# Kernel optimization log

Hardware: AMD Instinct MI355X
Metric: run time of the kernel (lower is better)

Reference implementation:

```python
import jax, jax.numpy as jnp
import numpy as np

N = 100000
E = 1600000
EPS = 1e-5
NEG_SLOPE = 0.01


def _leaky(x):
    return jnp.where(x > 0, x, NEG_SLOPE * x)


def _conv2d(x, w, b):
    # x: [N,Cin,H,W], w: [Cout,Cin,kh,kw], VALID padding, stride 1
    y = jax.lax.conv_general_dilated(x, w, (1, 1), 'VALID',
                                     dimension_numbers=('NCHW', 'OIHW', 'NCHW'))
    return y + b[None, :, None, None]


def _bn(x, g, b, m, v):
    # eval-mode BatchNorm1d over feature dim
    return (x - m) * (g / jnp.sqrt(v + EPS)) + b


def setup_inputs() -> dict:
    key = jax.random.key(0)
    ks = jax.random.split(key, 64)
    d = {}
    d['inputs'] = jax.random.normal(ks[0], (N, 1, 100, 5), dtype=jnp.float32)
    d['edge_index'] = jax.random.randint(ks[1], (2, E), 0, N, dtype=jnp.int32)
    # CNN encoder params (x=10)
    d['cw1'] = 0.1 * jax.random.normal(ks[2], (10, 1, 3, 3), dtype=jnp.float32)
    d['cb1'] = jnp.zeros((10,), jnp.float32)
    d['cw2'] = 0.1 * jax.random.normal(ks[3], (20, 10, 3, 2), dtype=jnp.float32)
    d['cb2'] = jnp.zeros((20,), jnp.float32)
    d['cw3'] = 0.1 * jax.random.normal(ks[4], (1, 20, 3, 2), dtype=jnp.float32)
    d['cb3'] = jnp.zeros((1,), jnp.float32)
    dims = [94, 128, 128, 64, 64, 16]
    for i in range(5):
        fi, fo = dims[i], dims[i + 1]
        k = 8 + 4 * i
        d[f'gw{i+1}'] = jax.random.normal(ks[k], (fi, fo), jnp.float32) / np.sqrt(fi)
        d[f'gb{i+1}'] = jnp.zeros((fo,), jnp.float32)
        d[f'bn{i+1}_g'] = 1.0 + 0.1 * jax.random.normal(ks[k + 1], (fo,), jnp.float32)
        d[f'bn{i+1}_b'] = 0.1 * jax.random.normal(ks[k + 2], (fo,), jnp.float32)
        d[f'bn{i+1}_m'] = 0.1 * jax.random.normal(ks[k + 3], (fo,), jnp.float32)
        d[f'bn{i+1}_v'] = jax.random.uniform(ks[k + 3], (fo,), jnp.float32, 0.5, 1.5)
    return d


def reference(inputs, edge_index,
              cw1, cb1, cw2, cb2, cw3, cb3,
              gw1, gb1, gw2, gb2, gw3, gb3, gw4, gb4, gw5, gb5,
              bn1_g, bn1_b, bn1_m, bn1_v,
              bn2_g, bn2_b, bn2_m, bn2_v,
              bn3_g, bn3_b, bn3_m, bn3_v,
              bn4_g, bn4_b, bn4_m, bn4_v,
              bn5_g, bn5_b, bn5_m, bn5_v):
    n = inputs.shape[0]
    # --- GCN normalization (self-loops + symmetric deg^-1/2) ---
    loops = jnp.arange(n, dtype=edge_index.dtype)
    src = jnp.concatenate([edge_index[0], loops])
    dst = jnp.concatenate([edge_index[1], loops])
    deg = jax.ops.segment_sum(jnp.ones_like(src, dtype=jnp.float32), dst, num_segments=n)
    dinv = jnp.where(deg > 0, jax.lax.rsqrt(deg), 0.0)
    norm = dinv[src] * dinv[dst]  # [E+N]

    def gcn(h, w, b):
        m = (h @ w)[src] * norm[:, None]
        return jax.ops.segment_sum(m, dst, num_segments=n) + b

    # --- CNN encoder (dropout identity in eval) ---
    h = _conv2d(inputs, cw1, cb1)
    h = _leaky(h)
    h = _conv2d(h, cw2, cb2)
    h = _leaky(h)
    h = _conv2d(h, cw3, cb3)  # [N,1,94,1]
    h = jnp.tanh(h.reshape(-1, 94))

    h = jnp.tanh(_bn(gcn(h, gw1, gb1), bn1_g, bn1_b, bn1_m, bn1_v))
    h = jnp.tanh(_bn(gcn(h, gw2, gb2), bn2_g, bn2_b, bn2_m, bn2_v))
    h = jnp.tanh(_bn(gcn(h, gw3, gb3), bn3_g, bn3_b, bn3_m, bn3_v))
    h = jnp.tanh(_bn(gcn(h, gw4, gb4), bn4_g, bn4_b, bn4_m, bn4_v))
    h = _bn(gcn(h, gw5, gb5), bn5_g, bn5_b, bn5_m, bn5_v)
    return jax.nn.softmax(h, axis=1)
```

## Files before the change

### kernel.cpp

```cpp
#include <hip/hip_runtime.h>
#include <math.h>

namespace {

constexpr int NN = 100000;
constexpr int NE = 1600000;
constexpr float EPS = 1e-5f;

__device__ __forceinline__ float leaky(float x) { return fmaxf(x, 0.01f * x); }
__device__ __forceinline__ float ffma(float a, float b, float c) { return __builtin_fmaf(a, b, c); }


__global__ __launch_bounds__(256) void k_init(int* __restrict__ deg, int* __restrict__ counter, int n) {
  int i = blockIdx.x * 256 + threadIdx.x;
  if (i < n) deg[i] = 1;
  if (i == 0) counter[0] = 0;
}

__global__ __launch_bounds__(256) void k_count(const int* __restrict__ dst, int* __restrict__ deg, int e) {
  int i = blockIdx.x * 256 + threadIdx.x;
  if (i < e) atomicAdd(&deg[dst[i]], 1);
}

__global__ __launch_bounds__(256) void k_alloc(const int* __restrict__ deg, float* __restrict__ dinv,
                                               int* __restrict__ offsets, int* __restrict__ cursor,
                                               int* __restrict__ counter, int n) {
  int i = blockIdx.x * 256 + threadIdx.x;
  int lane = threadIdx.x & 63;
  int c = 0;
  if (i < n) {
    int d = deg[i];
    dinv[i] = rsqrtf((float)d);
    c = d - 1;
  }
  int v = c;
#pragma unroll
  for (int s = 1; s < 64; s <<= 1) {
    int t = __shfl_up(v, s, 64);
    if (lane >= s) v += t;
  }
  int total = __shfl(v, 63, 64);
  int base = 0;
  if (lane == 63) base = atomicAdd(counter, total);
  base = __shfl(base, 63, 64);
  if (i < n) {
    int off = base + v - c;
    offsets[i] = off;
    cursor[i] = off;
  }
}

__global__ __launch_bounds__(256) void k_fill(const int* __restrict__ src, const int* __restrict__ dst,
                                              const float* __restrict__ dinv, int* __restrict__ cursor,
                                              int2* __restrict__ adj, int e) {
  int i = blockIdx.x * 256 + threadIdx.x;
  if (i < e) {
    int s = src[i], d = dst[i];
    int p = atomicAdd(&cursor[d], 1);
    adj[p] = make_int2(s, __float_as_int(dinv[s] * dinv[d]));
  }
}

__global__ __launch_bounds__(256) void k_padw1(const float* __restrict__ gw1, float* __restrict__ w1p) {
  int i = blockIdx.x * 256 + threadIdx.x;
  if (i < 96 * 128) w1p[i] = (i < 94 * 128) ? gw1[i] : 0.f;
}

struct BNParams {
  const float* bg[5];
  const float* bv[5];
  const float* gb[5];
  const float* bm[5];
  const float* bb[5];
};
__global__ __launch_bounds__(512) void k_bnprep(BNParams p, float* __restrict__ scale, float* __restrict__ shift) {
  int i = threadIdx.x;
  if (i >= 400) return;
  const int ends[5] = {128, 256, 320, 384, 400};
  int l = 0;
  while (i >= ends[l]) l++;
  int c = i - (l ? ends[l - 1] : 0);
  float sc = p.bg[l][c] * rsqrtf(p.bv[l][c] + EPS);
  scale[i] = sc;
  shift[i] = ffma(p.gb[l][c] - p.bm[l][c], sc, p.bb[l][c]);
}

__global__ __launch_bounds__(256, 4) void k_cnn(const float* __restrict__ x,
                                             const float* __restrict__ cw1, const float* __restrict__ cb1,
                                             const float* __restrict__ cw2, const float* __restrict__ cb2,
                                             const float* __restrict__ cw3, const float* __restrict__ cb3,
                                             float* __restrict__ H) {
  __shared__ __align__(16) float inb[2][500];
  __shared__ float c1[2][2940];
  __shared__ float part[2][2][2][98];

  int tid = threadIdx.x;
  int half = tid >> 7;
  int nt = tid & 127;
  int lane = tid & 63;
  int node = blockIdx.x * 2 + half;
  int co0 = __builtin_amdgcn_readfirstlane(((tid >> 6) & 1) * 10);

  for (int i = tid; i < 2 * 2 * 2 * 98; i += 256) ((float*)part)[i] = 0.f;

  if (nt < 125) {
    const float4* xp = (const float4*)(x + (size_t)node * 500);
    ((float4*)inb[half])[nt] = xp[nt];
  }
  __syncthreads();

  {
    const float* in = inb[half];
    float* c1p = c1[half];
    int h = nt;
    if (h < 98) {
      float xv[3][5];
#pragma unroll
      for (int kh = 0; kh < 3; kh++)
#pragma unroll
        for (int c = 0; c < 5; c++) xv[kh][c] = in[(h + kh) * 5 + c];
      float* rowp = c1p + h * 3;
#pragma unroll
      for (int co = 0; co < 10; co++) {
        float b = cb1[co];
        float a0 = b, a1 = b, a2 = b;
#pragma unroll
        for (int kh = 0; kh < 3; kh++)
#pragma unroll
          for (int kw = 0; kw < 3; kw++) {
            float wv = cw1[co * 9 + kh * 3 + kw];
            a0 = ffma(xv[kh][kw + 0], wv, a0);
            a1 = ffma(xv[kh][kw + 1], wv, a1);
            a2 = ffma(xv[kh][kw + 2], wv, a2);
          }
        rowp[co * 294 + 0] = leaky(a0);
        rowp[co * 294 + 1] = leaky(a1);
        rowp[co * 294 + 2] = leaky(a2);
      }
    }
  }
  __syncthreads();

  int hg = lane >> 1, w = lane & 1;
  int h0 = hg * 3;
  float acc[3][10];
#pragma unroll
  for (int a = 0; a < 3; a++)
#pragma unroll
    for (int c = 0; c < 10; c++) acc[a][c] = 0.f;
  {
    const float* c1p = c1[half];
#pragma unroll 1
    for (int ci = 0; ci < 10; ci++) {
      float r[5][2];
      const float* base = c1p + ci * 294 + h0 * 3 + w;
#pragma unroll
      for (int i = 0; i < 5; i++) {
        r[i][0] = base[i * 3];
        r[i][1] = base[i * 3 + 1];
      }
#pragma unroll
      for (int c = 0; c < 10; c++) {
        const float* wp = cw2 + (co0 + c) * 60 + ci * 6;
        float w0 = wp[0], w1 = wp[1], w2v = wp[2], w3v = wp[3], w4 = wp[4], w5 = wp[5];
#pragma unroll
        for (int hh = 0; hh < 3; hh++) {
          float t = acc[hh][c];
          t = ffma(r[hh][0],     w0,  t);
          t = ffma(r[hh][1],     w1,  t);
          t = ffma(r[hh + 1][0], w2v, t);
          t = ffma(r[hh + 1][1], w3v, t);
          t = ffma(r[hh + 2][0], w4,  t);
          t = ffma(r[hh + 2][1], w5,  t);
          acc[hh][c] = t;
        }
      }
    }
#pragma unroll
    for (int c = 0; c < 10; c++) {
      float b = cb2[co0 + c];
#pragma unroll
      for (int hh = 0; hh < 3; hh++) acc[hh][c] = leaky(acc[hh][c] + b);
    }
  }
  __syncthreads();

  {
    float* pp = &part[half][co0 == 0 ? 0 : 1][w][0];
#pragma unroll
    for (int kh = 0; kh < 3; kh++) {
      float ws[10];
#pragma unroll
      for (int c = 0; c < 10; c++) {
        float wa = cw3[(co0 + c) * 6 + kh * 2 + 0];
        float wb = cw3[(co0 + c) * 6 + kh * 2 + 1];
        ws[c] = w ? wb : wa;
      }
#pragma unroll
      for (int hh = 0; hh < 3; hh++) {
        float s = 0.f;
#pragma unroll
        for (int c = 0; c < 10; c++) s = ffma(acc[hh][c], ws[c], s);
        pp[h0 + hh - kh + 2] += s;
      }
      __syncthreads();
    }
  }

  {
    float* Hp = H + (size_t)node * 96;
    if (nt < 94) {
      float v = part[half][0][0][nt + 2] + part[half][0][1][nt + 2]
              + part[half][1][0][nt + 2] + part[half][1][1][nt + 2] + cb3[0];
      Hp[nt] = tanhf(v);
    } else if (nt < 96) {
      Hp[nt] = 0.f;
    }
  }
}

template <int K, int FO, int BN>
__global__ __launch_bounds__(256) void k_gemm(const float* __restrict__ A, const float* __restrict__ W,
                                              float* __restrict__ C, int M) {
  __shared__ float As[64][K + 1];
  __shared__ __align__(16) float Ws[K][BN];
  int tid = threadIdx.x;
  int row_base = blockIdx.x * 64;
  int col_base = blockIdx.y * BN;

  for (int idx = tid; idx < 64 * K; idx += 256) {
    int r = idx / K, k = idx - r * K;
    int row = row_base + r;
    As[r][k] = (row < M) ? A[(size_t)row * K + k] : 0.f;
  }
  for (int idx = tid; idx < K * BN; idx += 256) {
    int r = idx / BN, c = idx - r * BN;
    Ws[r][c] = W[r * FO + col_base + c];
  }
  __syncthreads();

  if constexpr (BN == 64) {
    int ty = tid >> 4, tx = tid & 15;
    float acc[4][4] = {};
#pragma unroll 4
    for (int k = 0; k < K; k++) {
      float a0 = As[ty * 4 + 0][k];
      float a1 = As[ty * 4 + 1][k];
      float a2 = As[ty * 4 + 2][k];
      float a3 = As[ty * 4 + 3][k];
      const float4 b = *(const float4*)&Ws[k][tx * 4];
      acc[0][0] = ffma(a0, b.x, acc[0][0]); acc[0][1] = ffma(a0, b.y, acc[0][1]);
      acc[0][2] = ffma(a0, b.z, acc[0][2]); acc[0][3] = ffma(a0, b.w, acc[0][3]);
      acc[1][0] = ffma(a1, b.x, acc[1][0]); acc[1][1] = ffma(a1, b.y, acc[1][1]);
      acc[1][2] = ffma(a1, b.z, acc[1][2]); acc[1][3] = ffma(a1, b.w, acc[1][3]);
      acc[2][0] = ffma(a2, b.x, acc[2][0]); acc[2][1] = ffma(a2, b.y, acc[2][1]);
      acc[2][2] = ffma(a2, b.z, acc[2][2]); acc[2][3] = ffma(a2, b.w, acc[2][3]);
      acc[3][0] = ffma(a3, b.x, acc[3][0]); acc[3][1] = ffma(a3, b.y, acc[3][1]);
      acc[3][2] = ffma(a3, b.z, acc[3][2]); acc[3][3] = ffma(a3, b.w, acc[3][3]);
    }
#pragma unroll
    for (int i = 0; i < 4; i++) {
      int row = row_base + ty * 4 + i;
      if (row < M) {
        float4 v = make_float4(acc[i][0], acc[i][1], acc[i][2], acc[i][3]);
        *(float4*)&C[(size_t)row * FO + col_base + tx * 4] = v;
      }
    }
  } else {
    int ty = tid >> 2, tx = tid & 3;
    float acc[4] = {};
#pragma unroll 4
    for (int k = 0; k < K; k++) {
      float a = As[ty][k];
      const float4 b = *(const float4*)&Ws[k][tx * 4];
      acc[0] = ffma(a, b.x, acc[0]); acc[1] = ffma(a, b.y, acc[1]);
      acc[2] = ffma(a, b.z, acc[2]); acc[3] = ffma(a, b.w, acc[3]);
    }
    int row = row_base + ty;
    if (row < M) *(float4*)&C[(size_t)row * FO + col_base + tx * 4] = make_float4(acc[0], acc[1], acc[2], acc[3]);
  }
}

template <int FO, bool SOFT>
__global__ __launch_bounds__(256) void k_agg(const float* __restrict__ XW,
                                             const int* __restrict__ offsets, const int* __restrict__ deg,
                                             const int2* __restrict__ adj,
                                             const float* __restrict__ dinv,
                                             const float* __restrict__ bnscale, const float* __restrict__ bnshift,
                                             int bnofs, float* __restrict__ out, int n) {
  constexpr int TPN = FO / 8;
  constexpr int NPB = 256 / TPN;
  int tid = threadIdx.x;
  int li = tid / TPN, c8 = (tid % TPN) * 8;
  int node = blockIdx.x * NPB + li;
  if (node >= n) return;

  float dv = dinv[node];
  float se = dv * dv;
  const float4* selfp = (const float4*)&XW[(size_t)node * FO + c8];
  float4 aL = selfp[0], aH = selfp[1];
  aL.x *= se; aL.y *= se; aL.z *= se; aL.w *= se;
  aH.x *= se; aH.y *= se; aH.z *= se; aH.w *= se;

  const int2* ap = adj + offsets[node];
  int cnt = deg[node] - 1;
  int e = 0;
  for (; e + 1 < cnt; e += 2) {
    int2 a0 = ap[e], a1 = ap[e + 1];
    float nm0 = __int_as_float(a0.y), nm1 = __int_as_float(a1.y);
    const float4* q0 = (const float4*)&XW[(size_t)a0.x * FO + c8];
    const float4* q1 = (const float4*)&XW[(size_t)a1.x * FO + c8];
    float4 v0 = q0[0], w0 = q0[1];
    float4 v1 = q1[0], w1 = q1[1];
    aL.x = ffma(v0.x, nm0, aL.x); aL.y = ffma(v0.y, nm0, aL.y);
    aL.z = ffma(v0.z, nm0, aL.z); aL.w = ffma(v0.w, nm0, aL.w);
    aH.x = ffma(w0.x, nm0, aH.x); aH.y = ffma(w0.y, nm0, aH.y);
    aH.z = ffma(w0.z, nm0, aH.z); aH.w = ffma(w0.w, nm0, aH.w);
    aL.x = ffma(v1.x, nm1, aL.x); aL.y = ffma(v1.y, nm1, aL.y);
    aL.z = ffma(v1.z, nm1, aL.z); aL.w = ffma(v1.w, nm1, aL.w);
    aH.x = ffma(w1.x, nm1, aH.x); aH.y = ffma(w1.y, nm1, aH.y);
    aH.z = ffma(w1.z, nm1, aH.z); aH.w = ffma(w1.w, nm1, aH.w);
  }
  if (e < cnt) {
    int2 a0 = ap[e];
    float nm0 = __int_as_float(a0.y);
    const float4* q0 = (const float4*)&XW[(size_t)a0.x * FO + c8];
    float4 v0 = q0[0], w0 = q0[1];
    aL.x = ffma(v0.x, nm0, aL.x); aL.y = ffma(v0.y, nm0, aL.y);
    aL.z = ffma(v0.z, nm0, aL.z); aL.w = ffma(v0.w, nm0, aL.w);
    aH.x = ffma(w0.x, nm0, aH.x); aH.y = ffma(w0.y, nm0, aH.y);
    aH.z = ffma(w0.z, nm0, aH.z); aH.w = ffma(w0.w, nm0, aH.w);
  }

  const float4 s4L = *(const float4*)&bnscale[bnofs + c8];
  const float4 s4H = *(const float4*)&bnscale[bnofs + c8 + 4];
  const float4 h4L = *(const float4*)&bnshift[bnofs + c8];
  const float4 h4H = *(const float4*)&bnshift[bnofs + c8 + 4];
  float r[8];
  r[0] = ffma(aL.x, s4L.x, h4L.x); r[1] = ffma(aL.y, s4L.y, h4L.y);
  r[2] = ffma(aL.z, s4L.z, h4L.z); r[3] = ffma(aL.w, s4L.w, h4L.w);
  r[4] = ffma(aH.x, s4H.x, h4H.x); r[5] = ffma(aH.y, s4H.y, h4H.y);
  r[6] = ffma(aH.z, s4H.z, h4H.z); r[7] = ffma(aH.w, s4H.w, h4H.w);

  float4 oL, oH;
  if constexpr (SOFT) {
    float mx = r[0];
#pragma unroll
    for (int i = 1; i < 8; i++) mx = fmaxf(mx, r[i]);
#pragma unroll
    for (int m = TPN / 2; m; m >>= 1) mx = fmaxf(mx, __shfl_xor(mx, m, TPN));
    float sm = 0.f;
#pragma unroll
    for (int i = 0; i < 8; i++) { r[i] = expf(r[i] - mx); sm += r[i]; }
#pragma unroll
    for (int m = TPN / 2; m; m >>= 1) sm += __shfl_xor(sm, m, TPN);
    float inv = 1.f / sm;
#pragma unroll
    for (int i = 0; i < 8; i++) r[i] *= inv;
  } else {
#pragma unroll
    for (int i = 0; i < 8; i++) r[i] = tanhf(r[i]);
  }
  oL = make_float4(r[0], r[1], r[2], r[3]);
  oH = make_float4(r[4], r[5], r[6], r[7]);
  float4* op = (float4*)&out[(size_t)node * FO + c8];
  op[0] = oL;
  op[1] = oH;
}

}

extern "C" void kernel_launch(void* const* d_in, const int* in_sizes, int n_in,
                              void* d_out, int out_size, void* d_ws, size_t ws_size,
                              hipStream_t stream) {
  const float* x   = (const float*)d_in[0];
  const int*   ei  = (const int*)d_in[1];
  const float* cw1 = (const float*)d_in[2];
  const float* cb1 = (const float*)d_in[3];
  const float* cw2 = (const float*)d_in[4];
  const float* cb2 = (const float*)d_in[5];
  const float* cw3 = (const float*)d_in[6];
  const float* cb3 = (const float*)d_in[7];
  const float *gw[5], *gb[5], *bng[5], *bnb[5], *bnm[5], *bnv[5];
  for (int l = 0; l < 5; l++) {
    gw[l]  = (const float*)d_in[8 + 6 * l + 0];
    gb[l]  = (const float*)d_in[8 + 6 * l + 1];
    bng[l] = (const float*)d_in[8 + 6 * l + 2];
    bnb[l] = (const float*)d_in[8 + 6 * l + 3];
    bnm[l] = (const float*)d_in[8 + 6 * l + 4];
    bnv[l] = (const float*)d_in[8 + 6 * l + 5];
  }
  const int* srcp = ei;
  const int* dstp = ei + NE;

  char* w = (char*)d_ws;
  auto alloc = [&](size_t bytes) { char* p = w; w += (bytes + 255) & ~255ULL; return p; };
  int*   deg     = (int*)alloc((size_t)NN * 4);
  int*   offsets = (int*)alloc((size_t)NN * 4);
  int*   cursor  = (int*)alloc((size_t)NN * 4);
  int*   counter = (int*)alloc(256);
  float* dinv    = (float*)alloc((size_t)NN * 4);
  int2*  adj     = (int2*)alloc((size_t)NE * 8);
  float* w1p     = (float*)alloc(96 * 128 * 4);
  float* bnscale = (float*)alloc(400 * 4);
  float* bnshift = (float*)alloc(400 * 4);
  float* bufA    = (float*)alloc((size_t)NN * 128 * 4);
  float* bufB    = (float*)alloc((size_t)NN * 128 * 4);
  float* bufC    = (float*)alloc((size_t)NN * 128 * 4);

  int nb_n = (NN + 255) / 256;
  int nb_e = (NE + 255) / 256;
  k_init<<<nb_n, 256, 0, stream>>>(deg, counter, NN);
  k_count<<<nb_e, 256, 0, stream>>>(dstp, deg, NE);
  k_alloc<<<nb_n, 256, 0, stream>>>(deg, dinv, offsets, cursor, counter, NN);
  k_fill<<<nb_e, 256, 0, stream>>>(srcp, dstp, dinv, cursor, adj, NE);
  k_padw1<<<48, 256, 0, stream>>>(gw[0], w1p);
  {
    BNParams bp;
    for (int l = 0; l < 5; l++) {
      bp.bg[l] = bng[l]; bp.bv[l] = bnv[l]; bp.gb[l] = gb[l];
      bp.bm[l] = bnm[l]; bp.bb[l] = bnb[l];
    }
    k_bnprep<<<1, 512, 0, stream>>>(bp, bnscale, bnshift);
  }

  k_cnn<<<NN / 2, 256, 0, stream>>>(x, cw1, cb1, cw2, cb2, cw3, cb3, bufA);

  int gx = (NN + 63) / 64;
  k_gemm<96, 128, 64><<<dim3(gx, 2), 256, 0, stream>>>(bufA, w1p, bufB, NN);
  k_agg<128, false><<<(NN + 15) / 16, 256, 0, stream>>>(bufB, offsets, deg, adj, dinv,
                                                        bnscale, bnshift, 0, bufC, NN);
  k_gemm<128, 128, 64><<<dim3(gx, 2), 256, 0, stream>>>(bufC, gw[1], bufB, NN);
  k_agg<128, false><<<(NN + 15) / 16, 256, 0, stream>>>(bufB, offsets, deg, adj, dinv,
                                                        bnscale, bnshift, 128, bufA, NN);
  k_gemm<128, 64, 64><<<dim3(gx, 1), 256, 0, stream>>>(bufA, gw[2], bufB, NN);
  k_agg<64, false><<<(NN + 31) / 32, 256, 0, stream>>>(bufB, offsets, deg, adj, dinv,
                                                       bnscale, bnshift, 256, bufC, NN);
  k_gemm<64, 64, 64><<<dim3(gx, 1), 256, 0, stream>>>(bufC, gw[3], bufB, NN);
  k_agg<64, false><<<(NN + 31) / 32, 256, 0, stream>>>(bufB, offsets, deg, adj, dinv,
                                                       bnscale, bnshift, 320, bufA, NN);
  k_gemm<64, 16, 16><<<dim3(gx, 1), 256, 0, stream>>>(bufA, gw[4], bufB, NN);
  k_agg<16, true><<<(NN + 127) / 128, 256, 0, stream>>>(bufB, offsets, deg, adj, dinv,
                                                        bnscale, bnshift, 384, (float*)d_out, NN);
}
```

Baseline: 1.433 ms.

## Aggregate before GEMM in first GCN layer and unroll edge loop by four

Uses linearity of the GCN layer to aggregate the 96-wide CNN features over neighbors first, then run the 96x128 GEMM with a fused BN+tanh epilogue. The sparse gather then moves 96 floats per edge instead of 128, and the separate aggregation for layer 1 is replaced by the epilogue. The generic aggregation kernel's edge loop is also unrolled by four to keep more gathers in flight. Floating-point summation order changes slightly.

```diff
diff --git a/kernel.cpp b/kernel.cpp
--- a/kernel.cpp
+++ b/kernel.cpp
@@ -219,9 +219,12 @@
   }
 }
 
-template <int K, int FO, int BN>
+template <int K, int FO, int BN, bool EPI = false>
 __global__ __launch_bounds__(256) void k_gemm(const float* __restrict__ A, const float* __restrict__ W,
-                                              float* __restrict__ C, int M) {
+                                              float* __restrict__ C, int M,
+                                              const float* __restrict__ bns = nullptr,
+                                              const float* __restrict__ bnh = nullptr,
+                                              int bnofs = 0) {
   __shared__ float As[64][K + 1];
   __shared__ __align__(16) float Ws[K][BN];
   int tid = threadIdx.x;
@@ -258,11 +261,24 @@
       acc[3][0] = ffma(a3, b.x, acc[3][0]); acc[3][1] = ffma(a3, b.y, acc[3][1]);
       acc[3][2] = ffma(a3, b.z, acc[3][2]); acc[3][3] = ffma(a3, b.w, acc[3][3]);
     }
+    float4 s4, h4;
+    if constexpr (EPI) {
+      s4 = *(const float4*)&bns[bnofs + col_base + tx * 4];
+      h4 = *(const float4*)&bnh[bnofs + col_base + tx * 4];
+    }
 #pragma unroll
     for (int i = 0; i < 4; i++) {
       int row = row_base + ty * 4 + i;
       if (row < M) {
-        float4 v = make_float4(acc[i][0], acc[i][1], acc[i][2], acc[i][3]);
+        float4 v;
+        if constexpr (EPI) {
+          v.x = tanhf(ffma(acc[i][0], s4.x, h4.x));
+          v.y = tanhf(ffma(acc[i][1], s4.y, h4.y));
+          v.z = tanhf(ffma(acc[i][2], s4.z, h4.z));
+          v.w = tanhf(ffma(acc[i][3], s4.w, h4.w));
+        } else {
+          v = make_float4(acc[i][0], acc[i][1], acc[i][2], acc[i][3]);
+        }
         *(float4*)&C[(size_t)row * FO + col_base + tx * 4] = v;
       }
     }
@@ -279,6 +295,63 @@
     int row = row_base + ty;
     if (row < M) *(float4*)&C[(size_t)row * FO + col_base + tx * 4] = make_float4(acc[0], acc[1], acc[2], acc[3]);
   }
+}
+
+__global__ __launch_bounds__(256) void k_agg96(const float* __restrict__ Hm,
+                                               const int* __restrict__ offsets, const int* __restrict__ deg,
+                                               const int2* __restrict__ adj,
+                                               const float* __restrict__ dinv,
+                                               float* __restrict__ out, int n) {
+  int tid = threadIdx.x;
+  int li = tid >> 3, c12 = (tid & 7) * 12;
+  int node = blockIdx.x * 32 + li;
+  if (node >= n) return;
+
+  float dv = dinv[node];
+  float se = dv * dv;
+  const float4* sp = (const float4*)&Hm[(size_t)node * 96 + c12];
+  float4 a0 = sp[0], a1 = sp[1], a2 = sp[2];
+  a0.x *= se; a0.y *= se; a0.z *= se; a0.w *= se;
+  a1.x *= se; a1.y *= se; a1.z *= se; a1.w *= se;
+  a2.x *= se; a2.y *= se; a2.z *= se; a2.w *= se;
+
+  const int2* ap = adj + offsets[node];
+  int cnt = deg[node] - 1;
+  int e = 0;
+  for (; e + 1 < cnt; e += 2) {
+    int2 e0 = ap[e], e1 = ap[e + 1];
+    float n0 = __int_as_float(e0.y), n1 = __int_as_float(e1.y);
+    const float4* q0 = (const float4*)&Hm[(size_t)e0.x * 96 + c12];
+    const float4* q1 = (const float4*)&Hm[(size_t)e1.x * 96 + c12];
+    float4 u0 = q0[0], u1 = q0[1], u2 = q0[2];
+    float4 v0 = q1[0], v1 = q1[1], v2 = q1[2];
+    a0.x = ffma(u0.x, n0, a0.x); a0.y = ffma(u0.y, n0, a0.y);
+    a0.z = ffma(u0.z, n0, a0.z); a0.w = ffma(u0.w, n0, a0.w);
+    a1.x = ffma(u1.x, n0, a1.x); a1.y = ffma(u1.y, n0, a1.y);
+    a1.z = ffma(u1.z, n0, a1.z); a1.w = ffma(u1.w, n0, a1.w);
+    a2.x = ffma(u2.x, n0, a2.x); a2.y = ffma(u2.y, n0, a2.y);
+    a2.z = ffma(u2.z, n0, a2.z); a2.w = ffma(u2.w, n0, a2.w);
+    a0.x = ffma(v0.x, n1, a0.x); a0.y = ffma(v0.y, n1, a0.y);
+    a0.z = ffma(v0.z, n1, a0.z); a0.w = ffma(v0.w, n1, a0.w);
+    a1.x = ffma(v1.x, n1, a1.x); a1.y = ffma(v1.y, n1, a1.y);
+    a1.z = ffma(v1.z, n1, a1.z); a1.w = ffma(v1.w, n1, a1.w);
+    a2.x = ffma(v2.x, n1, a2.x); a2.y = ffma(v2.y, n1, a2.y);
+    a2.z = ffma(v2.z, n1, a2.z); a2.w = ffma(v2.w, n1, a2.w);
+  }
+  if (e < cnt) {
+    int2 e0 = ap[e];
+    float n0 = __int_as_float(e0.y);
+    const float4* q0 = (const float4*)&Hm[(size_t)e0.x * 96 + c12];
+    float4 u0 = q0[0], u1 = q0[1], u2 = q0[2];
+    a0.x = ffma(u0.x, n0, a0.x); a0.y = ffma(u0.y, n0, a0.y);
+    a0.z = ffma(u0.z, n0, a0.z); a0.w = ffma(u0.w, n0, a0.w);
+    a1.x = ffma(u1.x, n0, a1.x); a1.y = ffma(u1.y, n0, a1.y);
+    a1.z = ffma(u1.z, n0, a1.z); a1.w = ffma(u1.w, n0, a1.w);
+    a2.x = ffma(u2.x, n0, a2.x); a2.y = ffma(u2.y, n0, a2.y);
+    a2.z = ffma(u2.z, n0, a2.z); a2.w = ffma(u2.w, n0, a2.w);
+  }
+  float4* op = (float4*)&out[(size_t)node * 96 + c12];
+  op[0] = a0; op[1] = a1; op[2] = a2;
 }
 
 template <int FO, bool SOFT>
@@ -305,32 +378,25 @@
   const int2* ap = adj + offsets[node];
   int cnt = deg[node] - 1;
   int e = 0;
-  for (; e + 1 < cnt; e += 2) {
-    int2 a0 = ap[e], a1 = ap[e + 1];
-    float nm0 = __int_as_float(a0.y), nm1 = __int_as_float(a1.y);
-    const float4* q0 = (const float4*)&XW[(size_t)a0.x * FO + c8];
-    const float4* q1 = (const float4*)&XW[(size_t)a1.x * FO + c8];
-    float4 v0 = q0[0], w0 = q0[1];
-    float4 v1 = q1[0], w1 = q1[1];
-    aL.x = ffma(v0.x, nm0, aL.x); aL.y = ffma(v0.y, nm0, aL.y);
-    aL.z = ffma(v0.z, nm0, aL.z); aL.w = ffma(v0.w, nm0, aL.w);
-    aH.x = ffma(w0.x, nm0, aH.x); aH.y = ffma(w0.y, nm0, aH.y);
-    aH.z = ffma(w0.z, nm0, aH.z); aH.w = ffma(w0.w, nm0, aH.w);
-    aL.x = ffma(v1.x, nm1, aL.x); aL.y = ffma(v1.y, nm1, aL.y);
-    aL.z = ffma(v1.z, nm1, aL.z); aL.w = ffma(v1.w, nm1, aL.w);
-    aH.x = ffma(w1.x, nm1, aH.x); aH.y = ffma(w1.y, nm1, aH.y);
-    aH.z = ffma(w1.z, nm1, aH.z); aH.w = ffma(w1.w, nm1, aH.w);
-  }
-  if (e < cnt) {
+#define EDGE_STEP(AA)                                                        \
+  {                                                                          \
+    float nm = __int_as_float((AA).y);                                       \
+    const float4* q = (const float4*)&XW[(size_t)(AA).x * FO + c8];          \
+    float4 v = q[0], w = q[1];                                               \
+    aL.x = ffma(v.x, nm, aL.x); aL.y = ffma(v.y, nm, aL.y);                  \
+    aL.z = ffma(v.z, nm, aL.z); aL.w = ffma(v.w, nm, aL.w);                  \
+    aH.x = ffma(w.x, nm, aH.x); aH.y = ffma(w.y, nm, aH.y);                  \
+    aH.z = ffma(w.z, nm, aH.z); aH.w = ffma(w.w, nm, aH.w);                  \
+  }
+  for (; e + 3 < cnt; e += 4) {
+    int2 a0 = ap[e], a1 = ap[e + 1], a2 = ap[e + 2], a3 = ap[e + 3];
+    EDGE_STEP(a0); EDGE_STEP(a1); EDGE_STEP(a2); EDGE_STEP(a3);
+  }
+  for (; e < cnt; e++) {
     int2 a0 = ap[e];
-    float nm0 = __int_as_float(a0.y);
-    const float4* q0 = (const float4*)&XW[(size_t)a0.x * FO + c8];
-    float4 v0 = q0[0], w0 = q0[1];
-    aL.x = ffma(v0.x, nm0, aL.x); aL.y = ffma(v0.y, nm0, aL.y);
-    aL.z = ffma(v0.z, nm0, aL.z); aL.w = ffma(v0.w, nm0, aL.w);
-    aH.x = ffma(w0.x, nm0, aH.x); aH.y = ffma(w0.y, nm0, aH.y);
-    aH.z = ffma(w0.z, nm0, aH.z); aH.w = ffma(w0.w, nm0, aH.w);
-  }
+    EDGE_STEP(a0);
+  }
+#undef EDGE_STEP
 
   const float4 s4L = *(const float4*)&bnscale[bnofs + c8];
   const float4 s4H = *(const float4*)&bnscale[bnofs + c8 + 4];
@@ -427,9 +493,8 @@
   k_cnn<<<NN / 2, 256, 0, stream>>>(x, cw1, cb1, cw2, cb2, cw3, cb3, bufA);
 
   int gx = (NN + 63) / 64;
-  k_gemm<96, 128, 64><<<dim3(gx, 2), 256, 0, stream>>>(bufA, w1p, bufB, NN);
-  k_agg<128, false><<<(NN + 15) / 16, 256, 0, stream>>>(bufB, offsets, deg, adj, dinv,
-                                                        bnscale, bnshift, 0, bufC, NN);
+  k_agg96<<<(NN + 31) / 32, 256, 0, stream>>>(bufA, offsets, deg, adj, dinv, bufB, NN);
+  k_gemm<96, 128, 64, true><<<dim3(gx, 2), 256, 0, stream>>>(bufB, w1p, bufC, NN, bnscale, bnshift, 0);
   k_gemm<128, 128, 64><<<dim3(gx, 2), 256, 0, stream>>>(bufC, gw[1], bufB, NN);
   k_agg<128, false><<<(NN + 15) / 16, 256, 0, stream>>>(bufB, offsets, deg, adj, dinv,
                                                         bnscale, bnshift, 128, bufA, NN);
```

Result: faster. 1.398 ms (-2.4%).
